# Optimization experiments

Hardware: AMD Instinct MI355X
Metric: run time of the kernel (lower is better)

## Reference

```python
import jax, jax.numpy as jnp
import numpy as np

EMB_DIM = 2048
USER_DIM = 256
NUM_EXPERTS = 64
TOP_K = 8
N_TOKENS = 16384


def setup_inputs() -> dict:
    key = jax.random.key(0)
    k_h, k_u, k_w = jax.random.split(key, 3)
    h = jax.random.normal(k_h, (N_TOKENS, EMB_DIM), dtype=jnp.float32)
    u = jax.random.normal(k_u, (N_TOKENS, USER_DIM), dtype=jnp.float32)
    # nn.Linear weight is [out, in]; we store transposed [in, out] for x @ W
    W = jax.random.normal(k_w, (EMB_DIM + USER_DIM, NUM_EXPERTS), dtype=jnp.float32) * (1.0 / np.sqrt(EMB_DIM + USER_DIM))
    b = jnp.zeros((NUM_EXPERTS,), dtype=jnp.float32)
    return {"h": h, "u": u, "W": W, "b": b}


def reference(h, u, W, b):
    # gate logits: [N, E]
    g = jnp.concatenate([h, u], axis=-1) @ W + b
    w = jax.nn.softmax(g, axis=-1)
    # top-k mask + renormalize (top_k < num_experts)
    _, top_idx = jax.lax.top_k(w, TOP_K)                       # [N, k]
    mask = jax.nn.one_hot(top_idx, NUM_EXPERTS, dtype=w.dtype).sum(axis=-2)  # [N, E]
    w = w * mask
    w = w / (w.sum(axis=-1, keepdims=True) + 1e-9)
    return w
```

## Files before the change

kernel.cpp:

```cpp
#include <hip/hip_runtime.h>

#define EMB 2048
#define UDIM 256
#define KTOT 2304
#define NE 64
#define TOPK 8
#define SSH 6144
#define STEPB 12288
#define KSPL 8
#define SPS 9
#define SLICEB (SPS * STEPB)
#define NTOK 16384
#define PART_OFF (1 << 20)

typedef __attribute__((ext_vector_type(8))) short short8;
typedef __attribute__((ext_vector_type(4))) float f32x4;
typedef __attribute__((ext_vector_type(4))) unsigned int u32x4;

__device__ __forceinline__ unsigned short bf16h(float x) {
  unsigned uu = __builtin_bit_cast(unsigned, x);
  return (unsigned short)((uu + 0x7FFFu + ((uu >> 16) & 1u)) >> 16);
}
__device__ __forceinline__ float bf2f(unsigned short s) {
  return __builtin_bit_cast(float, ((unsigned)s) << 16);
}

__device__ __forceinline__ unsigned cvtpk(float a, float b) {
  unsigned r;
  asm("v_cvt_pk_bf16_f32 %0, %1, %2" : "=v"(r) : "v"(a), "v"(b));
  return r;
}

__global__ __launch_bounds__(256)
void prep_w(const float* __restrict__ W, unsigned short* __restrict__ wb) {
  const int flat = blockIdx.x * 256 + threadIdx.x;
  const int k = flat >> 6;
  const int n = flat & 63;
  const float w = W[flat];
  const unsigned short h0 = bf16h(w);
  const float r1 = w - bf2f(h0);
  const unsigned short h1 = bf16h(r1);
  const float r2 = r1 - bf2f(h1);
  const unsigned short h2 = bf16h(r2);

  const int s = k >> 5;
  const int kk = k & 31;
  const int lane = (kk >> 3) * 16 + (n & 15);
  const int j = kk & 7;
  const int nt = n >> 4;
  const size_t base = (size_t)s * SSH + ((size_t)nt * 64 + lane) * 8 + j;
  wb[base] = h0;
  wb[base + 2048] = h1;
  wb[base + 4096] = h2;
}

__global__ __launch_bounds__(512, 2)
void gate_split(const float* __restrict__ h, const float* __restrict__ u,
                const unsigned short* __restrict__ wb,
                float* __restrict__ partial) {
  __shared__ __align__(1024) char lds[SLICEB];

  const int tid = threadIdx.x;
  const int lane = tid & 63;
  const int wid = __builtin_amdgcn_readfirstlane(tid >> 6);
  const int kq = blockIdx.x >> 5;
  const int bb = blockIdx.x & 31;
  const int mm = lane & 15;
  const int q8 = (lane >> 4) * 8;

  const char* src = (const char*)wb + (size_t)kq * SLICEB + (size_t)lane * 16;
  for (int j = wid; j < SPS * 12; j += 8)
    __builtin_amdgcn_global_load_lds(
        (const __attribute__((address_space(1))) unsigned int*)(src + (size_t)j * 1024),
        (__attribute__((address_space(3))) unsigned int*)(lds + (size_t)j * 1024),
        16, 0, 0);
  __syncthreads();

  const bool tail = (kq == KSPL - 1);
  const char* lb = lds + (size_t)lane * 16;

#pragma unroll 1
  for (int tt = 0; tt < 4; ++tt) {
    const int tile = (bb * 8 + wid) * 4 + tt;
    const int token = tile * 16 + mm;
    const float* hb = h + (size_t)token * EMB + kq * (SPS * 32) + q8;
    const float* ht = h + (size_t)token * EMB + 2016 + q8;
    const float* ub = u + (size_t)token * UDIM + q8;

    f32x4 A[2 * SPS];
#pragma unroll
    for (int s = 0; s < SPS; ++s) {
      const float* bs = !tail ? (hb + s * 32)
                              : (s == 0 ? ht : (ub + (s - 1) * 32));
      A[2 * s] = *(const f32x4*)bs;
      A[2 * s + 1] = *(const f32x4*)(bs + 4);
    }

    f32x4 acc[4];
#pragma unroll
    for (int nt = 0; nt < 4; ++nt) acc[nt] = 0.f;

#pragma unroll
    for (int s = 0; s < SPS; ++s) {
      short8 Bv[12];
#pragma unroll
      for (int q = 0; q < 12; ++q)
        Bv[q] = *(const short8*)(lb + (size_t)s * STEPB + q * 1024);

      const f32x4 c0 = A[2 * s], c1 = A[2 * s + 1];
      const float xs[8] = {c0[0], c0[1], c0[2], c0[3],
                           c1[0], c1[1], c1[2], c1[3]};
      u32x4 W0, W1, W2;
#pragma unroll
      for (int k2 = 0; k2 < 4; ++k2) {
        const float a = xs[2 * k2], bbv = xs[2 * k2 + 1];
        const unsigned p0 = cvtpk(a, bbv);
        const float a1 = a - __builtin_bit_cast(float, p0 << 16);
        const float b1 = bbv - __builtin_bit_cast(float, p0 & 0xFFFF0000u);
        const unsigned p1 = cvtpk(a1, b1);
        const float a2 = a1 - __builtin_bit_cast(float, p1 << 16);
        const float b2 = b1 - __builtin_bit_cast(float, p1 & 0xFFFF0000u);
        const unsigned p2 = cvtpk(a2, b2);
        W0[k2] = p0; W1[k2] = p1; W2[k2] = p2;
      }
      const short8 A0 = __builtin_bit_cast(short8, W0);
      const short8 A1 = __builtin_bit_cast(short8, W1);
      const short8 A2 = __builtin_bit_cast(short8, W2);

#pragma unroll
      for (int nt = 0; nt < 4; ++nt) {
        acc[nt] = __builtin_amdgcn_mfma_f32_16x16x32_bf16(A0, Bv[0 + nt], acc[nt], 0, 0, 0);
        acc[nt] = __builtin_amdgcn_mfma_f32_16x16x32_bf16(A0, Bv[4 + nt], acc[nt], 0, 0, 0);
        acc[nt] = __builtin_amdgcn_mfma_f32_16x16x32_bf16(A1, Bv[0 + nt], acc[nt], 0, 0, 0);
        acc[nt] = __builtin_amdgcn_mfma_f32_16x16x32_bf16(A1, Bv[4 + nt], acc[nt], 0, 0, 0);
        acc[nt] = __builtin_amdgcn_mfma_f32_16x16x32_bf16(A0, Bv[8 + nt], acc[nt], 0, 0, 0);
        acc[nt] = __builtin_amdgcn_mfma_f32_16x16x32_bf16(A2, Bv[0 + nt], acc[nt], 0, 0, 0);
      }
    }

    const int rowb = (lane >> 4) * 4;
#pragma unroll
    for (int nt = 0; nt < 4; ++nt)
#pragma unroll
      for (int r = 0; r < 4; ++r)
        partial[((size_t)kq * NTOK + tile * 16 + rowb + r) * NE + nt * 16 + mm] =
            acc[nt][r];
  }
}

__global__ __launch_bounds__(256)
void finalize(const float* __restrict__ partial, const float* __restrict__ b,
              float* __restrict__ out) {
  const int tid = threadIdx.x;
  const int lane = tid & 63;
  const int wid = tid >> 6;
  const int tok0 = blockIdx.x * 64;
  const float bias = b[lane];

#pragma unroll 1
  for (int tt = 0; tt < 16; ++tt) {
    const int t = tok0 + wid * 16 + tt;
    float g = bias;
#pragma unroll
    for (int s = 0; s < KSPL; ++s)
      g += partial[((size_t)s * NTOK + t) * NE + lane];

    float m = g;
#pragma unroll
    for (int off = 32; off > 0; off >>= 1)
      m = fmaxf(m, __shfl_xor(m, off));
    float pexp = __expf(g - m);
    float sum = pexp;
#pragma unroll
    for (int off = 32; off > 0; off >>= 1)
      sum += __shfl_xor(sum, off);
    const float pn = pexp / sum;

    float vv = pn;
    float topsum = 0.f;
    int sel = 0;
    for (int r = 0; r < TOPK; ++r) {
      float mv = vv;
      int mi = lane;
#pragma unroll
      for (int off = 32; off > 0; off >>= 1) {
        const float ov = __shfl_xor(mv, off);
        const int oi = __shfl_xor(mi, off);
        if (ov > mv || (ov == mv && oi < mi)) { mv = ov; mi = oi; }
      }
      topsum += mv;
      if (lane == mi) { sel = 1; vv = -1.f; }
    }

    out[(size_t)t * NE + lane] = sel ? pn / (topsum + 1e-9f) : 0.f;
  }
}

extern "C" void kernel_launch(void* const* d_in, const int* in_sizes, int n_in,
                              void* d_out, int out_size, void* d_ws, size_t ws_size,
                              hipStream_t stream) {
  const float* h = (const float*)d_in[0];
  const float* u = (const float*)d_in[1];
  const float* W = (const float*)d_in[2];
  const float* b = (const float*)d_in[3];
  float* out = (float*)d_out;

  unsigned short* wb = (unsigned short*)d_ws;
  float* partial = (float*)((char*)d_ws + PART_OFF);

  hipLaunchKernelGGL(prep_w, dim3(KTOT * NE / 256), dim3(256), 0, stream, W, wb);
  hipLaunchKernelGGL(gate_split, dim3(KSPL * 32), dim3(512), 0, stream,
                     h, u, wb, partial);
  hipLaunchKernelGGL(finalize, dim3(NTOK / 64), dim3(256), 0, stream,
                     partial, b, out);
}
```

Baseline: 296.2 us.

## Software-pipeline A-tile loads across token tiles and spread finalize over more blocks

The gate GEMM loop over four token tiles is unrolled into a double-buffered schedule. The next tile's global activation loads are issued midway through the current tile's MFMA steps, with sched_barriers to keep that ordering, so load latency is hidden behind compute. The finalize kernel now gives one token per wave, raising the block count from 256 to 4096 for more parallelism. The cost is higher register pressure from two A buffers, which could spill or reduce occupancy.

```diff
diff --git a/kernel.cpp b/kernel.cpp
--- a/kernel.cpp
+++ b/kernel.cpp
@@ -78,16 +78,17 @@
 
   const bool tail = (kq == KSPL - 1);
   const char* lb = lds + (size_t)lane * 16;
-
-#pragma unroll 1
-  for (int tt = 0; tt < 4; ++tt) {
-    const int tile = (bb * 8 + wid) * 4 + tt;
+  const int tb = (bb * 8 + wid) * 4;
+
+  f32x4 acc[4];
+#pragma unroll
+  for (int nt = 0; nt < 4; ++nt) acc[nt] = 0.f;
+
+  auto aload = [&](int tile, f32x4* A) {
     const int token = tile * 16 + mm;
     const float* hb = h + (size_t)token * EMB + kq * (SPS * 32) + q8;
     const float* ht = h + (size_t)token * EMB + 2016 + q8;
     const float* ub = u + (size_t)token * UDIM + q8;
-
-    f32x4 A[2 * SPS];
 #pragma unroll
     for (int s = 0; s < SPS; ++s) {
       const float* bs = !tail ? (hb + s * 32)
@@ -95,57 +96,77 @@
       A[2 * s] = *(const f32x4*)bs;
       A[2 * s + 1] = *(const f32x4*)(bs + 4);
     }
-
-    f32x4 acc[4];
-#pragma unroll
-    for (int nt = 0; nt < 4; ++nt) acc[nt] = 0.f;
-
-#pragma unroll
-    for (int s = 0; s < SPS; ++s) {
-      short8 Bv[12];
-#pragma unroll
-      for (int q = 0; q < 12; ++q)
-        Bv[q] = *(const short8*)(lb + (size_t)s * STEPB + q * 1024);
-
-      const f32x4 c0 = A[2 * s], c1 = A[2 * s + 1];
-      const float xs[8] = {c0[0], c0[1], c0[2], c0[3],
-                           c1[0], c1[1], c1[2], c1[3]};
-      u32x4 W0, W1, W2;
-#pragma unroll
-      for (int k2 = 0; k2 < 4; ++k2) {
-        const float a = xs[2 * k2], bbv = xs[2 * k2 + 1];
-        const unsigned p0 = cvtpk(a, bbv);
-        const float a1 = a - __builtin_bit_cast(float, p0 << 16);
-        const float b1 = bbv - __builtin_bit_cast(float, p0 & 0xFFFF0000u);
-        const unsigned p1 = cvtpk(a1, b1);
-        const float a2 = a1 - __builtin_bit_cast(float, p1 << 16);
-        const float b2 = b1 - __builtin_bit_cast(float, p1 & 0xFFFF0000u);
-        const unsigned p2 = cvtpk(a2, b2);
-        W0[k2] = p0; W1[k2] = p1; W2[k2] = p2;
-      }
-      const short8 A0 = __builtin_bit_cast(short8, W0);
-      const short8 A1 = __builtin_bit_cast(short8, W1);
-      const short8 A2 = __builtin_bit_cast(short8, W2);
-
-#pragma unroll
-      for (int nt = 0; nt < 4; ++nt) {
-        acc[nt] = __builtin_amdgcn_mfma_f32_16x16x32_bf16(A0, Bv[0 + nt], acc[nt], 0, 0, 0);
-        acc[nt] = __builtin_amdgcn_mfma_f32_16x16x32_bf16(A0, Bv[4 + nt], acc[nt], 0, 0, 0);
-        acc[nt] = __builtin_amdgcn_mfma_f32_16x16x32_bf16(A1, Bv[0 + nt], acc[nt], 0, 0, 0);
-        acc[nt] = __builtin_amdgcn_mfma_f32_16x16x32_bf16(A1, Bv[4 + nt], acc[nt], 0, 0, 0);
-        acc[nt] = __builtin_amdgcn_mfma_f32_16x16x32_bf16(A0, Bv[8 + nt], acc[nt], 0, 0, 0);
-        acc[nt] = __builtin_amdgcn_mfma_f32_16x16x32_bf16(A2, Bv[0 + nt], acc[nt], 0, 0, 0);
-      }
-    }
-
+  };
+
+  auto stepf = [&](const f32x4* A, int s) {
+    short8 Bv[12];
+#pragma unroll
+    for (int q = 0; q < 12; ++q)
+      Bv[q] = *(const short8*)(lb + (size_t)s * STEPB + q * 1024);
+
+    const f32x4 c0 = A[2 * s], c1 = A[2 * s + 1];
+    const float xs[8] = {c0[0], c0[1], c0[2], c0[3],
+                         c1[0], c1[1], c1[2], c1[3]};
+    u32x4 W0, W1, W2;
+#pragma unroll
+    for (int k2 = 0; k2 < 4; ++k2) {
+      const float a = xs[2 * k2], bbv = xs[2 * k2 + 1];
+      const unsigned p0 = cvtpk(a, bbv);
+      const float a1 = a - __builtin_bit_cast(float, p0 << 16);
+      const float b1 = bbv - __builtin_bit_cast(float, p0 & 0xFFFF0000u);
+      const unsigned p1 = cvtpk(a1, b1);
+      const float a2 = a1 - __builtin_bit_cast(float, p1 << 16);
+      const float b2 = b1 - __builtin_bit_cast(float, p1 & 0xFFFF0000u);
+      const unsigned p2 = cvtpk(a2, b2);
+      W0[k2] = p0; W1[k2] = p1; W2[k2] = p2;
+    }
+    const short8 A0 = __builtin_bit_cast(short8, W0);
+    const short8 A1 = __builtin_bit_cast(short8, W1);
+    const short8 A2 = __builtin_bit_cast(short8, W2);
+
+#pragma unroll
+    for (int nt = 0; nt < 4; ++nt) {
+      acc[nt] = __builtin_amdgcn_mfma_f32_16x16x32_bf16(A0, Bv[0 + nt], acc[nt], 0, 0, 0);
+      acc[nt] = __builtin_amdgcn_mfma_f32_16x16x32_bf16(A0, Bv[4 + nt], acc[nt], 0, 0, 0);
+      acc[nt] = __builtin_amdgcn_mfma_f32_16x16x32_bf16(A1, Bv[0 + nt], acc[nt], 0, 0, 0);
+      acc[nt] = __builtin_amdgcn_mfma_f32_16x16x32_bf16(A1, Bv[4 + nt], acc[nt], 0, 0, 0);
+      acc[nt] = __builtin_amdgcn_mfma_f32_16x16x32_bf16(A0, Bv[8 + nt], acc[nt], 0, 0, 0);
+      acc[nt] = __builtin_amdgcn_mfma_f32_16x16x32_bf16(A2, Bv[0 + nt], acc[nt], 0, 0, 0);
+    }
+  };
+
+  auto steps = [&](const f32x4* A, int s0, int s1) {
+#pragma unroll
+    for (int s = s0; s < s1; ++s) stepf(A, s);
+  };
+
+  auto store = [&](int tile) {
     const int rowb = (lane >> 4) * 4;
 #pragma unroll
-    for (int nt = 0; nt < 4; ++nt)
+    for (int nt = 0; nt < 4; ++nt) {
 #pragma unroll
       for (int r = 0; r < 4; ++r)
         partial[((size_t)kq * NTOK + tile * 16 + rowb + r) * NE + nt * 16 + mm] =
             acc[nt][r];
-  }
+      acc[nt] = 0.f;
+    }
+  };
+
+  f32x4 Aa[2 * SPS], Ab[2 * SPS];
+  aload(tb + 0, Aa);
+  steps(Aa, 0, 4);
+  aload(tb + 1, Ab);
+  __builtin_amdgcn_sched_barrier(0);
+  steps(Aa, 4, SPS);  store(tb + 0);
+  steps(Ab, 0, 4);
+  aload(tb + 2, Aa);
+  __builtin_amdgcn_sched_barrier(0);
+  steps(Ab, 4, SPS);  store(tb + 1);
+  steps(Aa, 0, 4);
+  aload(tb + 3, Ab);
+  __builtin_amdgcn_sched_barrier(0);
+  steps(Aa, 4, SPS);  store(tb + 2);
+  steps(Ab, 0, SPS);  store(tb + 3);
 }
 
 __global__ __launch_bounds__(256)
@@ -153,47 +174,43 @@
               float* __restrict__ out) {
   const int tid = threadIdx.x;
   const int lane = tid & 63;
-  const int wid = tid >> 6;
-  const int tok0 = blockIdx.x * 64;
+  const int wv = tid >> 6;
+  const int t = blockIdx.x * 4 + wv;
   const float bias = b[lane];
 
-#pragma unroll 1
-  for (int tt = 0; tt < 16; ++tt) {
-    const int t = tok0 + wid * 16 + tt;
-    float g = bias;
-#pragma unroll
-    for (int s = 0; s < KSPL; ++s)
-      g += partial[((size_t)s * NTOK + t) * NE + lane];
-
-    float m = g;
-#pragma unroll
-    for (int off = 32; off > 0; off >>= 1)
-      m = fmaxf(m, __shfl_xor(m, off));
-    float pexp = __expf(g - m);
-    float sum = pexp;
-#pragma unroll
-    for (int off = 32; off > 0; off >>= 1)
-      sum += __shfl_xor(sum, off);
-    const float pn = pexp / sum;
-
-    float vv = pn;
-    float topsum = 0.f;
-    int sel = 0;
-    for (int r = 0; r < TOPK; ++r) {
-      float mv = vv;
-      int mi = lane;
-#pragma unroll
-      for (int off = 32; off > 0; off >>= 1) {
-        const float ov = __shfl_xor(mv, off);
-        const int oi = __shfl_xor(mi, off);
-        if (ov > mv || (ov == mv && oi < mi)) { mv = ov; mi = oi; }
-      }
-      topsum += mv;
-      if (lane == mi) { sel = 1; vv = -1.f; }
-    }
-
-    out[(size_t)t * NE + lane] = sel ? pn / (topsum + 1e-9f) : 0.f;
+  float g = bias;
+#pragma unroll
+  for (int s = 0; s < KSPL; ++s)
+    g += partial[((size_t)s * NTOK + t) * NE + lane];
+
+  float m = g;
+#pragma unroll
+  for (int off = 32; off > 0; off >>= 1)
+    m = fmaxf(m, __shfl_xor(m, off));
+  float pexp = __expf(g - m);
+  float sum = pexp;
+#pragma unroll
+  for (int off = 32; off > 0; off >>= 1)
+    sum += __shfl_xor(sum, off);
+  const float pn = pexp / sum;
+
+  float vv = pn;
+  float topsum = 0.f;
+  int sel = 0;
+  for (int r = 0; r < TOPK; ++r) {
+    float mv = vv;
+    int mi = lane;
+#pragma unroll
+    for (int off = 32; off > 0; off >>= 1) {
+      const float ov = __shfl_xor(mv, off);
+      const int oi = __shfl_xor(mi, off);
+      if (ov > mv || (ov == mv && oi < mi)) { mv = ov; mi = oi; }
+    }
+    topsum += mv;
+    if (lane == mi) { sel = 1; vv = -1.f; }
   }
+
+  out[(size_t)t * NE + lane] = sel ? pn / (topsum + 1e-9f) : 0.f;
 }
 
 extern "C" void kernel_launch(void* const* d_in, const int* in_sizes, int n_in,
@@ -211,6 +228,6 @@
   hipLaunchKernelGGL(prep_w, dim3(KTOT * NE / 256), dim3(256), 0, stream, W, wb);
   hipLaunchKernelGGL(gate_split, dim3(KSPL * 32), dim3(512), 0, stream,
                      h, u, wb, partial);
-  hipLaunchKernelGGL(finalize, dim3(NTOK / 64), dim3(256), 0, stream,
+  hipLaunchKernelGGL(finalize, dim3(NTOK / 4), dim3(256), 0, stream,
                      partial, b, out);
 }
```

After: 243.1 us. -17.9%, faster.
